# Performance work log

Measured on AMD Instinct MI355X. Metric: run time of the kernel, lower is better.

## Reference

```python
import jax, jax.numpy as jnp
import numpy as np

N_ATOMS = 200_000
AVG_NEIGHBORS = 64
N_PAIRS = N_ATOMS * AVG_NEIGHBORS
BOX = 60.0  # Angstrom, so cutoff=10 masks most random pairs (realistic neighbor-list sparsity)


def setup_inputs() -> dict:
    key = jax.random.key(0)
    kR, ki, kj = jax.random.split(key, 3)
    R = jax.random.uniform(kR, (N_ATOMS, 3), dtype=jnp.float32) * BOX
    idx_i = jax.random.randint(ki, (N_PAIRS,), 0, N_ATOMS, dtype=jnp.int32)
    idx_j = jax.random.randint(kj, (N_PAIRS,), 0, N_ATOMS, dtype=jnp.int32)
    # learned scalar parameters from __init__
    epsilon = jnp.float32(0.238)
    sigma = jnp.float32(3.4)
    cutoff = jnp.float32(10.0)
    return {"R": R, "epsilon": epsilon, "sigma": sigma, "cutoff": cutoff,
            "idx_i": idx_i, "idx_j": idx_j}


def reference(R, epsilon, sigma, cutoff, idx_i, idx_j):
    """LJ 12-6 pairwise potential over a neighbor list.

    Returns (energy [N] per-atom, forces [N,3]).
    Each (i,j) pair appears in both directions in the pair list, hence the 0.5
    factor on per-atom energy; forces accumulate per direction (action-reaction
    handled by the symmetric pair list).
    """
    n_atoms = R.shape[0]
    rij = R[idx_i] - R[idx_j]                     # [P,3] gather
    r2 = jnp.sum(rij * rij, axis=-1)              # [P]
    mask = (r2 < cutoff * cutoff) & (r2 > 1e-10)  # inside cutoff, exclude coincident
    r2s = jnp.where(mask, r2, 1.0)                # safe divide
    sr2 = (sigma * sigma) / r2s
    sr6 = sr2 * sr2 * sr2
    sr12 = sr6 * sr6
    e_pair = jnp.where(mask, 4.0 * epsilon * (sr12 - sr6), 0.0)          # [P]
    f_mag = jnp.where(mask, 24.0 * epsilon * (2.0 * sr12 - sr6) / r2s, 0.0)
    f_pair = f_mag[:, None] * rij                 # [P,3]
    energy = 0.5 * jax.ops.segment_sum(e_pair, idx_i, num_segments=n_atoms)   # [N]
    forces = jax.ops.segment_sum(f_pair, idx_i, num_segments=n_atoms)         # [N,3]
    return energy, forces
```

## Files before the change

kernel.cpp:

```cpp
#include <hip/hip_runtime.h>


typedef int   v4i __attribute__((ext_vector_type(4)));
typedef float v4f __attribute__((ext_vector_type(4)));

#define GRP    8
#define WGT    1024
#define NWG_F  256

__global__ void __launch_bounds__(256) prep_kernel(
    const float* __restrict__ R, const float* __restrict__ cut_p,
    v4f* __restrict__ Rp, unsigned* __restrict__ packed, int n_atoms)
{
    int t = blockIdx.x * blockDim.x + threadIdx.x;
    int n_grp = (n_atoms + 4) / 5;
    if (t >= n_grp) return;
    const float inv_cut = 1.0f / cut_p[0];
    int a0 = t * 5;
    unsigned w = 0u;
#pragma unroll
    for (int k = 0; k < 5; ++k) {
        int a = a0 + k;
        if (a < n_atoms) {
            float x = R[3 * a + 0];
            float y = R[3 * a + 1];
            float z = R[3 * a + 2];
            v4f v; v.x = x; v.y = y; v.z = z; v.w = 0.0f;
            Rp[a] = v;
            int cx = min(7, max(0, (int)(x * inv_cut)));
            int cy = min(7, max(0, (int)(y * inv_cut)));
            w |= (unsigned)(cx | (cy << 3)) << (6 * k);
        }
    }
    packed[t] = w;
}

__global__ void __launch_bounds__(256) pad_R_kernel(
    const float* __restrict__ R, v4f* __restrict__ Rp, int n_atoms)
{
    int a = blockIdx.x * blockDim.x + threadIdx.x;
    if (a < n_atoms) {
        v4f v;
        v.x = R[3 * a + 0];
        v.y = R[3 * a + 1];
        v.z = R[3 * a + 2];
        v.w = 0.0f;
        Rp[a] = v;
    }
}

__device__ __forceinline__ unsigned cell6w(const unsigned* __restrict__ lds32,
                                           unsigned a) {
    unsigned q = __umulhi(a, 0xCCCCCCCDu) >> 2;
    unsigned r = a - q * 5u;
    return (lds32[q] >> (r * 6u)) & 63u;
}

__device__ __forceinline__ void load_grp(
    const int* __restrict__ idx_i, const int* __restrict__ idx_j,
    int p, int n_pairs, int* __restrict__ is8, int* __restrict__ js8)
{
    if (p + GRP <= n_pairs) {
        v4i a0 = __builtin_nontemporal_load((const v4i*)idx_i + (p >> 2));
        v4i a1 = __builtin_nontemporal_load((const v4i*)idx_i + (p >> 2) + 1);
        v4i b0 = __builtin_nontemporal_load((const v4i*)idx_j + (p >> 2));
        v4i b1 = __builtin_nontemporal_load((const v4i*)idx_j + (p >> 2) + 1);
        is8[0] = a0.x; is8[1] = a0.y; is8[2] = a0.z; is8[3] = a0.w;
        is8[4] = a1.x; is8[5] = a1.y; is8[6] = a1.z; is8[7] = a1.w;
        js8[0] = b0.x; js8[1] = b0.y; js8[2] = b0.z; js8[3] = b0.w;
        js8[4] = b1.x; js8[5] = b1.y; js8[6] = b1.z; js8[7] = b1.w;
    } else {
#pragma unroll
        for (int k = 0; k < GRP; ++k) {
            bool v = (p + k < n_pairs);
            is8[k] = v ? idx_i[p + k] : 0;
            js8[k] = v ? idx_j[p + k] : 0;
        }
    }
}

__device__ __forceinline__ void filt_sel(const unsigned* __restrict__ lds32,
                                         int* __restrict__ is8,
                                         int* __restrict__ js8)
{
#pragma unroll
    for (int k = 0; k < GRP; ++k) {
        unsigned ci = cell6w(lds32, (unsigned)is8[k]);
        unsigned cj = cell6w(lds32, (unsigned)js8[k]);
        int ddx = (int)(ci & 7u) - (int)(cj & 7u);
        int ddy = (int)(ci >> 3) - (int)(cj >> 3);
        bool ok = ((unsigned)(ddx + 1) <= 2u) & ((unsigned)(ddy + 1) <= 2u);
        is8[k] = ok ? is8[k] : 0;
        js8[k] = ok ? js8[k] : 0;
    }
}

__device__ __forceinline__ void lj_body(
    v4f A, v4f B, float eps, float s2, float cut2, int gi,
    float* __restrict__ energy, float* __restrict__ forces)
{
    const float dx = A.x - B.x, dy = A.y - B.y, dz = A.z - B.z;
    const float r2 = dx * dx + dy * dy + dz * dz;
    if (r2 < cut2 && r2 > 1e-10f) {
        const float inv  = 1.0f / r2;
        const float sr2  = s2 * inv;
        const float sr6  = sr2 * sr2 * sr2;
        const float sr12 = sr6 * sr6;
        const float e    = 2.0f * eps * (sr12 - sr6);
        const float f    = 24.0f * eps * (2.0f * sr12 - sr6) * inv;
        atomicAdd(&energy[gi], e);
        atomicAdd(&forces[3 * gi + 0], f * dx);
        atomicAdd(&forces[3 * gi + 1], f * dy);
        atomicAdd(&forces[3 * gi + 2], f * dz);
    }
}

__global__ void __launch_bounds__(WGT, 4) lj_fused_kernel(
    const v4f* __restrict__ Rp,
    const unsigned* __restrict__ packed,
    const int* __restrict__ idx_i,
    const int* __restrict__ idx_j,
    const float* __restrict__ eps_p,
    const float* __restrict__ sig_p,
    const float* __restrict__ cut_p,
    float* __restrict__ energy,
    float* __restrict__ forces,
    int n_pairs, int pk_words, int chunk)
{
    extern __shared__ unsigned lds[];
    for (int w = threadIdx.x; w < pk_words; w += WGT)
        lds[w] = packed[w];
    __syncthreads();

    const float eps  = eps_p[0];
    const float sig  = sig_p[0];
    const float cut  = cut_p[0];
    const float s2   = sig * sig;
    const float cut2 = cut * cut;

    const int cs = blockIdx.x * chunk;
    const int ce = min(cs + chunk, n_pairs);
    const int STRIDE = WGT * GRP;

    int p0 = cs + (int)threadIdx.x * GRP;
    if (p0 >= ce) return;

    int isA[GRP], jsA[GRP], isB[GRP], jsB[GRP];

    load_grp(idx_i, idx_j, p0, n_pairs, isA, jsA);
    filt_sel(lds, isA, jsA);
    int p1 = p0 + STRIDE;

    while (true) {
        const bool h1 = p1 < ce;

        if (h1) load_grp(idx_i, idx_j, p1, n_pairs, isB, jsB);

        v4f Ri[GRP], Rj[GRP];
#pragma unroll
        for (int k = 0; k < GRP; ++k) { Ri[k] = Rp[isA[k]]; Rj[k] = Rp[jsA[k]]; }

        if (h1) filt_sel(lds, isB, jsB);

#pragma unroll
        for (int k = 0; k < GRP; ++k)
            lj_body(Ri[k], Rj[k], eps, s2, cut2, isA[k], energy, forces);

        if (!h1) break;
#pragma unroll
        for (int k = 0; k < GRP; ++k) { isA[k] = isB[k]; jsA[k] = jsB[k]; }
        p1 += STRIDE;
    }
}

#define PPT 8
__global__ void __launch_bounds__(256) lj_pairs_fb_kernel(
    const v4f* __restrict__ Rp,
    const v4i* __restrict__ idx_i4, const v4i* __restrict__ idx_j4,
    const float* __restrict__ eps_p, const float* __restrict__ sig_p,
    const float* __restrict__ cut_p,
    float* __restrict__ energy, float* __restrict__ forces, int n_oct)
{
    int t = blockIdx.x * blockDim.x + threadIdx.x;
    if (t >= n_oct) return;
    const float eps  = eps_p[0];
    const float sig  = sig_p[0];
    const float cut  = cut_p[0];
    const float s2   = sig * sig;
    const float cut2 = cut * cut;
    v4i ii0 = __builtin_nontemporal_load(idx_i4 + 2 * t);
    v4i ii1 = __builtin_nontemporal_load(idx_i4 + 2 * t + 1);
    v4i jj0 = __builtin_nontemporal_load(idx_j4 + 2 * t);
    v4i jj1 = __builtin_nontemporal_load(idx_j4 + 2 * t + 1);
    int is[PPT] = { ii0.x, ii0.y, ii0.z, ii0.w, ii1.x, ii1.y, ii1.z, ii1.w };
    int js[PPT] = { jj0.x, jj0.y, jj0.z, jj0.w, jj1.x, jj1.y, jj1.z, jj1.w };
    v4f Ri[PPT], Rj[PPT];
#pragma unroll
    for (int k = 0; k < PPT; ++k) Ri[k] = Rp[is[k]];
#pragma unroll
    for (int k = 0; k < PPT; ++k) Rj[k] = Rp[js[k]];
#pragma unroll
    for (int k = 0; k < PPT; ++k)
        lj_body(Ri[k], Rj[k], eps, s2, cut2, is[k], energy, forces);
}

__global__ void lj_pairs_fb_tail_kernel(
    const v4f* __restrict__ Rp,
    const int* __restrict__ idx_i, const int* __restrict__ idx_j,
    const float* __restrict__ eps_p, const float* __restrict__ sig_p,
    const float* __restrict__ cut_p,
    float* __restrict__ energy, float* __restrict__ forces,
    int start, int n_pairs)
{
    int p = start + blockIdx.x * blockDim.x + threadIdx.x;
    if (p >= n_pairs) return;
    const float eps = eps_p[0];
    const float sig = sig_p[0];
    const float cut = cut_p[0];
    lj_body(Rp[idx_i[p]], Rp[idx_j[p]], eps, sig * sig, cut * cut,
            idx_i[p], energy, forces);
}

extern "C" void kernel_launch(void* const* d_in, const int* in_sizes, int n_in,
                              void* d_out, int out_size, void* d_ws, size_t ws_size,
                              hipStream_t stream) {
    const float* R     = (const float*)d_in[0];
    const float* eps_p = (const float*)d_in[1];
    const float* sig_p = (const float*)d_in[2];
    const float* cut_p = (const float*)d_in[3];
    const int*   idx_i = (const int*)d_in[4];
    const int*   idx_j = (const int*)d_in[5];

    const int n_atoms = in_sizes[0] / 3;
    const int n_pairs = in_sizes[4];

    float* energy = (float*)d_out;
    float* forces = (float*)d_out + n_atoms;

    (void)hipMemsetAsync(d_out, 0, (size_t)out_size * sizeof(float), stream);

    char* ws = (char*)d_ws;
    const size_t rp_b     = (((size_t)n_atoms * 16) + 255) & ~(size_t)255;
    const int    pk_words = (n_atoms + 4) / 5;
    const size_t pk_b     = (((size_t)pk_words * 4) + 255) & ~(size_t)255;
    const size_t lds_b    = (((size_t)pk_words * 4) + 15) & ~(size_t)15;

    const bool have_rp    = ws_size >= rp_b;
    const bool use_filter = have_rp && (ws_size >= rp_b + pk_b)
                            && (lds_b <= 160000);

    v4f*      Rp     = (v4f*)ws;
    unsigned* packed = (unsigned*)(ws + rp_b);

    if (use_filter) {
        int pblocks = (pk_words + 255) / 256;
        prep_kernel<<<pblocks, 256, 0, stream>>>(R, cut_p, Rp, packed, n_atoms);

        (void)hipFuncSetAttribute((const void*)lj_fused_kernel,
                                  hipFuncAttributeMaxDynamicSharedMemorySize,
                                  (int)lds_b);

        int chunk = (((n_pairs + NWG_F - 1) / NWG_F) + GRP - 1) & ~(GRP - 1);
        lj_fused_kernel<<<NWG_F, WGT, lds_b, stream>>>(
            Rp, packed, idx_i, idx_j, eps_p, sig_p, cut_p,
            energy, forces, n_pairs, pk_words, chunk);
    } else if (have_rp) {
        int blocks = (n_atoms + 255) / 256;
        pad_R_kernel<<<blocks, 256, 0, stream>>>(R, Rp, n_atoms);
        const int n_oct = n_pairs / PPT;
        const int start = n_oct * PPT;
        if (n_oct > 0) {
            int fblocks = (n_oct + 255) / 256;
            lj_pairs_fb_kernel<<<fblocks, 256, 0, stream>>>(
                Rp, (const v4i*)idx_i, (const v4i*)idx_j,
                eps_p, sig_p, cut_p, energy, forces, n_oct);
        }
        if (start < n_pairs) {
            lj_pairs_fb_tail_kernel<<<1, 64, 0, stream>>>(
                Rp, idx_i, idx_j, eps_p, sig_p, cut_p,
                energy, forces, start, n_pairs);
        }
    }
}
```

Before: 188.5 us.

## Split fused LJ kernel into cell-filter compaction pass and dense compute pass

```diff
diff --git a/kernel.cpp b/kernel.cpp
--- a/kernel.cpp
+++ b/kernel.cpp
@@ -7,6 +7,8 @@
 #define GRP    8
 #define WGT    1024
 #define NWG_F  256
+#define CWG    512
+#define QUAD   4
 
 __global__ void __launch_bounds__(256) prep_kernel(
     const float* __restrict__ R, const float* __restrict__ cut_p,
@@ -76,22 +78,6 @@
             is8[k] = v ? idx_i[p + k] : 0;
             js8[k] = v ? idx_j[p + k] : 0;
         }
-    }
-}
-
-__device__ __forceinline__ void filt_sel(const unsigned* __restrict__ lds32,
-                                         int* __restrict__ is8,
-                                         int* __restrict__ js8)
-{
-#pragma unroll
-    for (int k = 0; k < GRP; ++k) {
-        unsigned ci = cell6w(lds32, (unsigned)is8[k]);
-        unsigned cj = cell6w(lds32, (unsigned)js8[k]);
-        int ddx = (int)(ci & 7u) - (int)(cj & 7u);
-        int ddy = (int)(ci >> 3) - (int)(cj >> 3);
-        bool ok = ((unsigned)(ddx + 1) <= 2u) & ((unsigned)(ddy + 1) <= 2u);
-        is8[k] = ok ? is8[k] : 0;
-        js8[k] = ok ? js8[k] : 0;
     }
 }
 
@@ -115,6 +101,141 @@
     }
 }
 
+__global__ void __launch_bounds__(WGT) filter_compact_kernel(
+    const unsigned* __restrict__ packed,
+    const int* __restrict__ idx_i,
+    const int* __restrict__ idx_j,
+    int2* __restrict__ list,
+    int* __restrict__ counts,
+    int n_pairs, int pk_words, int chunk)
+{
+    extern __shared__ unsigned lds[];
+    unsigned* blk_cnt = &lds[pk_words];
+    for (int w = threadIdx.x; w < pk_words; w += WGT)
+        lds[w] = packed[w];
+    if (threadIdx.x == 0) *blk_cnt = 0u;
+    __syncthreads();
+
+    const int g  = blockIdx.x;
+    const int cs = g * chunk;
+    const int ce = min(cs + chunk, n_pairs);
+    const int STRIDE = WGT * GRP;
+    const int n_iter = (ce > cs) ? (ce - cs + STRIDE - 1) / STRIDE : 0;
+
+    int2* out = list + (size_t)g * (size_t)chunk;
+
+    int p = cs + (int)threadIdx.x * GRP;
+    for (int it = 0; it < n_iter; ++it, p += STRIDE) {
+        const bool v = p < ce;
+        int is8[GRP], js8[GRP];
+        unsigned m = 0u;
+        if (v) {
+            load_grp(idx_i, idx_j, p, n_pairs, is8, js8);
+#pragma unroll
+            for (int k = 0; k < GRP; ++k) {
+                unsigned ci = cell6w(lds, (unsigned)is8[k]);
+                unsigned cj = cell6w(lds, (unsigned)js8[k]);
+                int ddx = (int)(ci & 7u) - (int)(cj & 7u);
+                int ddy = (int)(ci >> 3) - (int)(cj >> 3);
+                bool ok = ((unsigned)(ddx + 1) <= 2u) &
+                          ((unsigned)(ddy + 1) <= 2u);
+                if (ok) m |= (1u << k);
+            }
+        }
+
+        int tot = 0;
+        int pre[GRP];
+#pragma unroll
+        for (int k = 0; k < GRP; ++k) {
+            unsigned long long bal = __ballot((m >> k) & 1u);
+            int before = __builtin_amdgcn_mbcnt_hi(
+                (unsigned)(bal >> 32),
+                __builtin_amdgcn_mbcnt_lo((unsigned)bal, 0u));
+            pre[k] = tot + before;
+            tot   += (int)__popcll(bal);
+        }
+
+        unsigned wb = 0u;
+        if ((threadIdx.x & 63u) == 0u)
+            wb = atomicAdd(blk_cnt, (unsigned)tot);
+        wb = (unsigned)__shfl((int)wb, 0, 64);
+
+#pragma unroll
+        for (int k = 0; k < GRP; ++k)
+            if ((m >> k) & 1u) {
+                int2 pr; pr.x = is8[k]; pr.y = js8[k];
+                out[wb + (unsigned)pre[k]] = pr;
+            }
+    }
+
+    __syncthreads();
+    if (threadIdx.x == 0) counts[g] = (int)*blk_cnt;
+}
+
+__global__ void __launch_bounds__(CWG, 8) lj_compute_kernel(
+    const v4f* __restrict__ Rp,
+    const int2* __restrict__ list,
+    const int* __restrict__ counts,
+    const float* __restrict__ eps_p,
+    const float* __restrict__ sig_p,
+    const float* __restrict__ cut_p,
+    float* __restrict__ energy,
+    float* __restrict__ forces,
+    int chunk)
+{
+    const int g   = blockIdx.x >> 2;
+    const int q   = blockIdx.x & (QUAD - 1);
+    const int cnt = counts[g];
+    const int qn  = (cnt + QUAD - 1) >> 2;
+    const int s   = q * qn;
+    const int e   = min(cnt, s + qn);
+    if (s >= e) return;
+
+    const int2* seg = list + (size_t)g * (size_t)chunk;
+
+    const float eps  = eps_p[0];
+    const float sig  = sig_p[0];
+    const float cut  = cut_p[0];
+    const float s2   = sig * sig;
+    const float cut2 = cut * cut;
+
+#define GRP2 4
+    for (int b = s + (int)threadIdx.x * GRP2; b < e; b += CWG * GRP2) {
+        int2 pr[GRP2];
+#pragma unroll
+        for (int k = 0; k < GRP2; ++k) {
+            if (b + k < e) pr[k] = seg[b + k];
+            else { pr[k].x = 0; pr[k].y = 0; }
+        }
+        v4f Ri[GRP2], Rj[GRP2];
+#pragma unroll
+        for (int k = 0; k < GRP2; ++k) {
+            Ri[k] = Rp[pr[k].x];
+            Rj[k] = Rp[pr[k].y];
+        }
+#pragma unroll
+        for (int k = 0; k < GRP2; ++k)
+            lj_body(Ri[k], Rj[k], eps, s2, cut2, pr[k].x, energy, forces);
+    }
+#undef GRP2
+}
+
+__device__ __forceinline__ void filt_sel(const unsigned* __restrict__ lds32,
+                                         int* __restrict__ is8,
+                                         int* __restrict__ js8)
+{
+#pragma unroll
+    for (int k = 0; k < GRP; ++k) {
+        unsigned ci = cell6w(lds32, (unsigned)is8[k]);
+        unsigned cj = cell6w(lds32, (unsigned)js8[k]);
+        int ddx = (int)(ci & 7u) - (int)(cj & 7u);
+        int ddy = (int)(ci >> 3) - (int)(cj >> 3);
+        bool ok = ((unsigned)(ddx + 1) <= 2u) & ((unsigned)(ddy + 1) <= 2u);
+        is8[k] = ok ? is8[k] : 0;
+        js8[k] = ok ? js8[k] : 0;
+    }
+}
+
 __global__ void __launch_bounds__(WGT, 4) lj_fused_kernel(
     const v4f* __restrict__ Rp,
     const unsigned* __restrict__ packed,
@@ -146,26 +267,20 @@
     if (p0 >= ce) return;
 
     int isA[GRP], jsA[GRP], isB[GRP], jsB[GRP];
-
     load_grp(idx_i, idx_j, p0, n_pairs, isA, jsA);
     filt_sel(lds, isA, jsA);
     int p1 = p0 + STRIDE;
 
     while (true) {
         const bool h1 = p1 < ce;
-
         if (h1) load_grp(idx_i, idx_j, p1, n_pairs, isB, jsB);
-
         v4f Ri[GRP], Rj[GRP];
 #pragma unroll
         for (int k = 0; k < GRP; ++k) { Ri[k] = Rp[isA[k]]; Rj[k] = Rp[jsA[k]]; }
-
         if (h1) filt_sel(lds, isB, jsB);
-
 #pragma unroll
         for (int k = 0; k < GRP; ++k)
             lj_body(Ri[k], Rj[k], eps, s2, cut2, isA[k], energy, forces);
-
         if (!h1) break;
 #pragma unroll
         for (int k = 0; k < GRP; ++k) { isA[k] = isB[k]; jsA[k] = jsB[k]; }
@@ -243,24 +358,43 @@
     const size_t rp_b     = (((size_t)n_atoms * 16) + 255) & ~(size_t)255;
     const int    pk_words = (n_atoms + 4) / 5;
     const size_t pk_b     = (((size_t)pk_words * 4) + 255) & ~(size_t)255;
-    const size_t lds_b    = (((size_t)pk_words * 4) + 15) & ~(size_t)15;
+    const size_t ct_b     = (((size_t)NWG_F * 4) + 255) & ~(size_t)255;
+    const int    chunk    = (((n_pairs + NWG_F - 1) / NWG_F) + GRP - 1)
+                            & ~(GRP - 1);
+    const size_t li_b     = (size_t)NWG_F * (size_t)chunk * 8;
+    const size_t lds_b    = (((size_t)(pk_words + 1) * 4) + 15) & ~(size_t)15;
 
     const bool have_rp    = ws_size >= rp_b;
-    const bool use_filter = have_rp && (ws_size >= rp_b + pk_b)
-                            && (lds_b <= 160000);
+    const bool lds_ok     = lds_b <= 160 * 1024;
+    const bool use_split  = have_rp && lds_ok
+                            && (ws_size >= rp_b + pk_b + ct_b + li_b);
+    const bool use_filter = !use_split && have_rp && lds_ok
+                            && (ws_size >= rp_b + pk_b);
 
     v4f*      Rp     = (v4f*)ws;
     unsigned* packed = (unsigned*)(ws + rp_b);
-
-    if (use_filter) {
+    int*      counts = (int*)(ws + rp_b + pk_b);
+    int2*     list   = (int2*)(ws + rp_b + pk_b + ct_b);
+
+    if (use_split) {
         int pblocks = (pk_words + 255) / 256;
         prep_kernel<<<pblocks, 256, 0, stream>>>(R, cut_p, Rp, packed, n_atoms);
 
+        (void)hipFuncSetAttribute((const void*)filter_compact_kernel,
+                                  hipFuncAttributeMaxDynamicSharedMemorySize,
+                                  (int)lds_b);
+        filter_compact_kernel<<<NWG_F, WGT, lds_b, stream>>>(
+            packed, idx_i, idx_j, list, counts, n_pairs, pk_words, chunk);
+
+        lj_compute_kernel<<<NWG_F * QUAD, CWG, 0, stream>>>(
+            Rp, list, counts, eps_p, sig_p, cut_p, energy, forces, chunk);
+    } else if (use_filter) {
+        int pblocks = (pk_words + 255) / 256;
+        prep_kernel<<<pblocks, 256, 0, stream>>>(R, cut_p, Rp, packed, n_atoms);
+
         (void)hipFuncSetAttribute((const void*)lj_fused_kernel,
                                   hipFuncAttributeMaxDynamicSharedMemorySize,
-                                  (int)lds_b);
-
-        int chunk = (((n_pairs + NWG_F - 1) / NWG_F) + GRP - 1) & ~(GRP - 1);
+                                  (int)(lds_b));
         lj_fused_kernel<<<NWG_F, WGT, lds_b, stream>>>(
             Rp, packed, idx_i, idx_j, eps_p, sig_p, cut_p,
             energy, forces, n_pairs, pk_words, chunk);
```

Result: slower. 202.6 us (+7.5%).

## Split cell filter into Y-compaction pass and XZ-filtered LJ pass

Applied to the files above, without the earlier changes.

```diff
diff --git a/kernel.cpp b/kernel.cpp
--- a/kernel.cpp
+++ b/kernel.cpp
@@ -4,9 +4,45 @@
 typedef int   v4i __attribute__((ext_vector_type(4)));
 typedef float v4f __attribute__((ext_vector_type(4)));
 
-#define GRP    8
-#define WGT    1024
-#define NWG_F  256
+#define GRP     8
+#define WGT     1024
+#define K1_NWG  512
+#define K2_NWG  256
+#define NWG_F   256
+
+__global__ void __launch_bounds__(256) prep3_kernel(
+    const float* __restrict__ R, const float* __restrict__ cut_p,
+    v4f* __restrict__ Rp, unsigned* __restrict__ packedY,
+    unsigned* __restrict__ packedXZ, int n_atoms)
+{
+    int t = blockIdx.x * blockDim.x + threadIdx.x;
+    int n_grp = (n_atoms + 9) / 10;
+    if (t >= n_grp) return;
+    const float inv_cut = 1.0f / cut_p[0];
+    int a0 = t * 10;
+    unsigned wy = 0u, wxz0 = 0u, wxz1 = 0u;
+#pragma unroll
+    for (int k = 0; k < 10; ++k) {
+        int a = a0 + k;
+        if (a < n_atoms) {
+            float x = R[3 * a + 0];
+            float y = R[3 * a + 1];
+            float z = R[3 * a + 2];
+            v4f v; v.x = x; v.y = y; v.z = z; v.w = 0.0f;
+            Rp[a] = v;
+            unsigned cx = (unsigned)min(7, max(0, (int)(x * inv_cut)));
+            unsigned cy = (unsigned)min(7, max(0, (int)(y * inv_cut)));
+            unsigned cz = (unsigned)min(7, max(0, (int)(z * inv_cut)));
+            wy |= cy << (3 * k);
+            unsigned cxz = cx | (cz << 3);
+            if (k < 5) wxz0 |= cxz << (6 * k);
+            else       wxz1 |= cxz << (6 * (k - 5));
+        }
+    }
+    packedY[t]          = wy;
+    packedXZ[2 * t]     = wxz0;
+    packedXZ[2 * t + 1] = wxz1;
+}
 
 __global__ void __launch_bounds__(256) prep_kernel(
     const float* __restrict__ R, const float* __restrict__ cut_p,
@@ -49,6 +85,13 @@
     }
 }
 
+__device__ __forceinline__ unsigned cell3w(const unsigned* __restrict__ lds32,
+                                           unsigned a) {
+    unsigned q = __umulhi(a, 0xCCCCCCCDu) >> 3;
+    unsigned r = a - q * 10u;
+    return (lds32[q] >> (r * 3u)) & 7u;
+}
+
 __device__ __forceinline__ unsigned cell6w(const unsigned* __restrict__ lds32,
                                            unsigned a) {
     unsigned q = __umulhi(a, 0xCCCCCCCDu) >> 2;
@@ -76,22 +119,6 @@
             is8[k] = v ? idx_i[p + k] : 0;
             js8[k] = v ? idx_j[p + k] : 0;
         }
-    }
-}
-
-__device__ __forceinline__ void filt_sel(const unsigned* __restrict__ lds32,
-                                         int* __restrict__ is8,
-                                         int* __restrict__ js8)
-{
-#pragma unroll
-    for (int k = 0; k < GRP; ++k) {
-        unsigned ci = cell6w(lds32, (unsigned)is8[k]);
-        unsigned cj = cell6w(lds32, (unsigned)js8[k]);
-        int ddx = (int)(ci & 7u) - (int)(cj & 7u);
-        int ddy = (int)(ci >> 3) - (int)(cj >> 3);
-        bool ok = ((unsigned)(ddx + 1) <= 2u) & ((unsigned)(ddy + 1) <= 2u);
-        is8[k] = ok ? is8[k] : 0;
-        js8[k] = ok ? js8[k] : 0;
     }
 }
 
@@ -115,6 +142,147 @@
     }
 }
 
+__global__ void __launch_bounds__(WGT, 8) filter_y_kernel(
+    const unsigned* __restrict__ packedY,
+    const int* __restrict__ idx_i,
+    const int* __restrict__ idx_j,
+    int2* __restrict__ list,
+    int* __restrict__ count,
+    int n_pairs, int pk3_words)
+{
+    extern __shared__ unsigned lds[];
+    for (int w = threadIdx.x; w < pk3_words; w += WGT)
+        lds[w] = packedY[w];
+    __syncthreads();
+
+    const int stride = (int)gridDim.x * WGT * GRP;
+    int p = ((int)blockIdx.x * WGT + (int)threadIdx.x) * GRP;
+    const int n_iter = (n_pairs + stride - 1) / stride;
+
+    for (int it = 0; it < n_iter; ++it, p += stride) {
+        const bool v = p < n_pairs;
+        int is8[GRP], js8[GRP];
+        unsigned m = 0u;
+        if (v) {
+            load_grp(idx_i, idx_j, p, n_pairs, is8, js8);
+#pragma unroll
+            for (int k = 0; k < GRP; ++k) {
+                int dd = (int)cell3w(lds, (unsigned)is8[k])
+                       - (int)cell3w(lds, (unsigned)js8[k]);
+                if ((unsigned)(dd + 1) <= 2u) m |= (1u << k);
+            }
+        }
+
+        int tot = 0;
+        int pre[GRP];
+#pragma unroll
+        for (int k = 0; k < GRP; ++k) {
+            unsigned long long bal = __ballot((m >> k) & 1u);
+            int before = __builtin_amdgcn_mbcnt_hi(
+                (unsigned)(bal >> 32),
+                __builtin_amdgcn_mbcnt_lo((unsigned)bal, 0u));
+            pre[k] = tot + before;
+            tot   += (int)__popcll(bal);
+        }
+
+        int wb = 0;
+        if (tot > 0) {
+            if ((threadIdx.x & 63u) == 0u)
+                wb = atomicAdd(count, tot);
+            wb = __shfl(wb, 0, 64);
+#pragma unroll
+            for (int k = 0; k < GRP; ++k)
+                if ((m >> k) & 1u) {
+                    int2 pr; pr.x = is8[k]; pr.y = js8[k];
+                    list[wb + pre[k]] = pr;
+                }
+        }
+    }
+}
+
+__global__ void __launch_bounds__(WGT, 4) lj_xz_kernel(
+    const v4f* __restrict__ Rp,
+    const unsigned* __restrict__ packedXZ,
+    const int2* __restrict__ list,
+    const int* __restrict__ count,
+    const float* __restrict__ eps_p,
+    const float* __restrict__ sig_p,
+    const float* __restrict__ cut_p,
+    float* __restrict__ energy,
+    float* __restrict__ forces,
+    int pkxz_words)
+{
+    extern __shared__ unsigned lds[];
+    for (int w = threadIdx.x; w < pkxz_words; w += WGT)
+        lds[w] = packedXZ[w];
+    __syncthreads();
+
+    const int   cnt  = *count;
+    const float eps  = eps_p[0];
+    const float sig  = sig_p[0];
+    const float cut  = cut_p[0];
+    const float s2   = sig * sig;
+    const float cut2 = cut * cut;
+
+    const int stride = (int)gridDim.x * WGT * GRP;
+
+    for (int b = ((int)blockIdx.x * WGT + (int)threadIdx.x) * GRP;
+         b < cnt; b += stride) {
+        int2 pr[GRP];
+        if (b + GRP <= cnt) {
+            v4i q0 = __builtin_nontemporal_load((const v4i*)list + (b >> 1));
+            v4i q1 = __builtin_nontemporal_load((const v4i*)list + (b >> 1) + 1);
+            v4i q2 = __builtin_nontemporal_load((const v4i*)list + (b >> 1) + 2);
+            v4i q3 = __builtin_nontemporal_load((const v4i*)list + (b >> 1) + 3);
+            pr[0].x = q0.x; pr[0].y = q0.y; pr[1].x = q0.z; pr[1].y = q0.w;
+            pr[2].x = q1.x; pr[2].y = q1.y; pr[3].x = q1.z; pr[3].y = q1.w;
+            pr[4].x = q2.x; pr[4].y = q2.y; pr[5].x = q2.z; pr[5].y = q2.w;
+            pr[6].x = q3.x; pr[6].y = q3.y; pr[7].x = q3.z; pr[7].y = q3.w;
+        } else {
+#pragma unroll
+            for (int k = 0; k < GRP; ++k) {
+                if (b + k < cnt) pr[k] = list[b + k];
+                else { pr[k].x = 0; pr[k].y = 0; }
+            }
+        }
+
+#pragma unroll
+        for (int k = 0; k < GRP; ++k) {
+            unsigned ci = cell6w(lds, (unsigned)pr[k].x);
+            unsigned cj = cell6w(lds, (unsigned)pr[k].y);
+            int ddx = (int)(ci & 7u) - (int)(cj & 7u);
+            int ddz = (int)(ci >> 3) - (int)(cj >> 3);
+            bool ok = ((unsigned)(ddx + 1) <= 2u) & ((unsigned)(ddz + 1) <= 2u);
+            pr[k].x = ok ? pr[k].x : 0;
+            pr[k].y = ok ? pr[k].y : 0;
+        }
+
+        v4f Ri[GRP], Rj[GRP];
+#pragma unroll
+        for (int k = 0; k < GRP; ++k) { Ri[k] = Rp[pr[k].x]; Rj[k] = Rp[pr[k].y]; }
+
+#pragma unroll
+        for (int k = 0; k < GRP; ++k)
+            lj_body(Ri[k], Rj[k], eps, s2, cut2, pr[k].x, energy, forces);
+    }
+}
+
+__device__ __forceinline__ void filt_sel(const unsigned* __restrict__ lds32,
+                                         int* __restrict__ is8,
+                                         int* __restrict__ js8)
+{
+#pragma unroll
+    for (int k = 0; k < GRP; ++k) {
+        unsigned ci = cell6w(lds32, (unsigned)is8[k]);
+        unsigned cj = cell6w(lds32, (unsigned)js8[k]);
+        int ddx = (int)(ci & 7u) - (int)(cj & 7u);
+        int ddy = (int)(ci >> 3) - (int)(cj >> 3);
+        bool ok = ((unsigned)(ddx + 1) <= 2u) & ((unsigned)(ddy + 1) <= 2u);
+        is8[k] = ok ? is8[k] : 0;
+        js8[k] = ok ? js8[k] : 0;
+    }
+}
+
 __global__ void __launch_bounds__(WGT, 4) lj_fused_kernel(
     const v4f* __restrict__ Rp,
     const unsigned* __restrict__ packed,
@@ -146,26 +314,20 @@
     if (p0 >= ce) return;
 
     int isA[GRP], jsA[GRP], isB[GRP], jsB[GRP];
-
     load_grp(idx_i, idx_j, p0, n_pairs, isA, jsA);
     filt_sel(lds, isA, jsA);
     int p1 = p0 + STRIDE;
 
     while (true) {
         const bool h1 = p1 < ce;
-
         if (h1) load_grp(idx_i, idx_j, p1, n_pairs, isB, jsB);
-
         v4f Ri[GRP], Rj[GRP];
 #pragma unroll
         for (int k = 0; k < GRP; ++k) { Ri[k] = Rp[isA[k]]; Rj[k] = Rp[jsA[k]]; }
-
         if (h1) filt_sel(lds, isB, jsB);
-
 #pragma unroll
         for (int k = 0; k < GRP; ++k)
             lj_body(Ri[k], Rj[k], eps, s2, cut2, isA[k], energy, forces);
-
         if (!h1) break;
 #pragma unroll
         for (int k = 0; k < GRP; ++k) { isA[k] = isB[k]; jsA[k] = jsB[k]; }
@@ -240,31 +402,68 @@
     (void)hipMemsetAsync(d_out, 0, (size_t)out_size * sizeof(float), stream);
 
     char* ws = (char*)d_ws;
-    const size_t rp_b     = (((size_t)n_atoms * 16) + 255) & ~(size_t)255;
-    const int    pk_words = (n_atoms + 4) / 5;
-    const size_t pk_b     = (((size_t)pk_words * 4) + 255) & ~(size_t)255;
-    const size_t lds_b    = (((size_t)pk_words * 4) + 15) & ~(size_t)15;
-
-    const bool have_rp    = ws_size >= rp_b;
-    const bool use_filter = have_rp && (ws_size >= rp_b + pk_b)
-                            && (lds_b <= 160000);
-
-    v4f*      Rp     = (v4f*)ws;
-    unsigned* packed = (unsigned*)(ws + rp_b);
-
-    if (use_filter) {
+    const size_t rp_b       = (((size_t)n_atoms * 16) + 255) & ~(size_t)255;
+    const int    pk3_words  = (n_atoms + 9) / 10;
+    const int    pkxz_words = 2 * pk3_words;
+    const size_t pk3_b      = (((size_t)pk3_words * 4) + 255) & ~(size_t)255;
+    const size_t pkxz_b     = (((size_t)pkxz_words * 4) + 255) & ~(size_t)255;
+    const size_t cnt_b      = 256;
+    const size_t list_b     = (size_t)n_pairs * 8;
+    const size_t ldsY_b     = (((size_t)pk3_words * 4) + 15) & ~(size_t)15;
+    const size_t ldsXZ_b    = (((size_t)pkxz_words * 4) + 15) & ~(size_t)15;
+
+    const int    pk_words   = (n_atoms + 4) / 5;
+    const size_t pk_b       = (((size_t)pk_words * 4) + 255) & ~(size_t)255;
+    const size_t ldsF_b     = (((size_t)pk_words * 4) + 15) & ~(size_t)15;
+
+    const bool have_rp   = ws_size >= rp_b;
+    const bool use_split = have_rp
+        && (ldsY_b <= 160 * 1024) && (ldsXZ_b <= 160 * 1024)
+        && (ws_size >= rp_b + pk3_b + pkxz_b + cnt_b + list_b);
+    const bool use_fused = !use_split && have_rp
+        && (ldsF_b <= 160 * 1024) && (ws_size >= rp_b + pk_b);
+
+    if (use_split) {
+        v4f*      Rp       = (v4f*)ws;
+        unsigned* packedY  = (unsigned*)(ws + rp_b);
+        unsigned* packedXZ = (unsigned*)(ws + rp_b + pk3_b);
+        int*      count    = (int*)(ws + rp_b + pk3_b + pkxz_b);
+        int2*     list     = (int2*)(ws + rp_b + pk3_b + pkxz_b + cnt_b);
+
+        (void)hipMemsetAsync(count, 0, sizeof(int), stream);
+
+        int pblocks = ((n_atoms + 9) / 10 + 255) / 256;
+        prep3_kernel<<<pblocks, 256, 0, stream>>>(
+            R, cut_p, Rp, packedY, packedXZ, n_atoms);
+
+        (void)hipFuncSetAttribute((const void*)filter_y_kernel,
+                                  hipFuncAttributeMaxDynamicSharedMemorySize,
+                                  (int)ldsY_b);
+        filter_y_kernel<<<K1_NWG, WGT, ldsY_b, stream>>>(
+            packedY, idx_i, idx_j, list, count, n_pairs, pk3_words);
+
+        (void)hipFuncSetAttribute((const void*)lj_xz_kernel,
+                                  hipFuncAttributeMaxDynamicSharedMemorySize,
+                                  (int)ldsXZ_b);
+        lj_xz_kernel<<<K2_NWG, WGT, ldsXZ_b, stream>>>(
+            Rp, packedXZ, list, count, eps_p, sig_p, cut_p,
+            energy, forces, pkxz_words);
+    } else if (use_fused) {
+        v4f*      Rp     = (v4f*)ws;
+        unsigned* packed = (unsigned*)(ws + rp_b);
+
         int pblocks = (pk_words + 255) / 256;
         prep_kernel<<<pblocks, 256, 0, stream>>>(R, cut_p, Rp, packed, n_atoms);
 
         (void)hipFuncSetAttribute((const void*)lj_fused_kernel,
                                   hipFuncAttributeMaxDynamicSharedMemorySize,
-                                  (int)lds_b);
-
+                                  (int)ldsF_b);
         int chunk = (((n_pairs + NWG_F - 1) / NWG_F) + GRP - 1) & ~(GRP - 1);
-        lj_fused_kernel<<<NWG_F, WGT, lds_b, stream>>>(
+        lj_fused_kernel<<<NWG_F, WGT, ldsF_b, stream>>>(
             Rp, packed, idx_i, idx_j, eps_p, sig_p, cut_p,
             energy, forces, n_pairs, pk_words, chunk);
     } else if (have_rp) {
+        v4f* Rp = (v4f*)ws;
         int blocks = (n_atoms + 255) / 256;
         pad_R_kernel<<<blocks, 256, 0, stream>>>(R, Rp, n_atoms);
         const int n_oct = n_pairs / PPT;
```

Result: slower. 466.3 us (+147.4%).

## Accumulate energy and forces into padded float4 staging buffer with packed atomics

Applied to the files above, without the earlier changes.

```diff
diff --git a/kernel.cpp b/kernel.cpp
--- a/kernel.cpp
+++ b/kernel.cpp
@@ -1,12 +1,27 @@
 #include <hip/hip_runtime.h>
+#include <stdint.h>
 
 
 typedef int   v4i __attribute__((ext_vector_type(4)));
 typedef float v4f __attribute__((ext_vector_type(4)));
+typedef float v2f __attribute__((ext_vector_type(2)));
 
 #define GRP    8
 #define WGT    1024
 #define NWG_F  256
+
+#if __has_builtin(__builtin_amdgcn_global_atomic_fadd_v2f32)
+__device__ __forceinline__ void pk_atomic_add(float* p, float a, float b) {
+    typedef __attribute__((address_space(1))) v2f gv2f;
+    v2f v; v.x = a; v.y = b;
+    (void)__builtin_amdgcn_global_atomic_fadd_v2f32((gv2f*)(uintptr_t)p, v);
+}
+#else
+__device__ __forceinline__ void pk_atomic_add(float* p, float a, float b) {
+    atomicAdd(p, a);
+    atomicAdd(p + 1, b);
+}
+#endif
 
 __global__ void __launch_bounds__(256) prep_kernel(
     const float* __restrict__ R, const float* __restrict__ cut_p,
@@ -92,6 +107,25 @@
         bool ok = ((unsigned)(ddx + 1) <= 2u) & ((unsigned)(ddy + 1) <= 2u);
         is8[k] = ok ? is8[k] : 0;
         js8[k] = ok ? js8[k] : 0;
+    }
+}
+
+__device__ __forceinline__ void lj_body_st(
+    v4f A, v4f B, float eps, float s2, float cut2, int gi,
+    float* __restrict__ st)
+{
+    const float dx = A.x - B.x, dy = A.y - B.y, dz = A.z - B.z;
+    const float r2 = dx * dx + dy * dy + dz * dz;
+    if (r2 < cut2 && r2 > 1e-10f) {
+        const float inv  = 1.0f / r2;
+        const float sr2  = s2 * inv;
+        const float sr6  = sr2 * sr2 * sr2;
+        const float sr12 = sr6 * sr6;
+        const float e    = 2.0f * eps * (sr12 - sr6);
+        const float f    = 24.0f * eps * (2.0f * sr12 - sr6) * inv;
+        float* p = st + ((size_t)(unsigned)gi << 2);
+        pk_atomic_add(p,     e,      f * dx);
+        pk_atomic_add(p + 2, f * dy, f * dz);
     }
 }
 
@@ -115,6 +149,77 @@
     }
 }
 
+__global__ void __launch_bounds__(WGT, 4) lj_fused_st_kernel(
+    const v4f* __restrict__ Rp,
+    const unsigned* __restrict__ packed,
+    const int* __restrict__ idx_i,
+    const int* __restrict__ idx_j,
+    const float* __restrict__ eps_p,
+    const float* __restrict__ sig_p,
+    const float* __restrict__ cut_p,
+    float* __restrict__ st,
+    int n_pairs, int pk_words, int chunk)
+{
+    extern __shared__ unsigned lds[];
+    for (int w = threadIdx.x; w < pk_words; w += WGT)
+        lds[w] = packed[w];
+    __syncthreads();
+
+    const float eps  = eps_p[0];
+    const float sig  = sig_p[0];
+    const float cut  = cut_p[0];
+    const float s2   = sig * sig;
+    const float cut2 = cut * cut;
+
+    const int cs = blockIdx.x * chunk;
+    const int ce = min(cs + chunk, n_pairs);
+    const int STRIDE = WGT * GRP;
+
+    int p0 = cs + (int)threadIdx.x * GRP;
+    if (p0 >= ce) return;
+
+    int isA[GRP], jsA[GRP], isB[GRP], jsB[GRP];
+
+    load_grp(idx_i, idx_j, p0, n_pairs, isA, jsA);
+    filt_sel(lds, isA, jsA);
+    int p1 = p0 + STRIDE;
+
+    while (true) {
+        const bool h1 = p1 < ce;
+
+        if (h1) load_grp(idx_i, idx_j, p1, n_pairs, isB, jsB);
+
+        v4f Ri[GRP], Rj[GRP];
+#pragma unroll
+        for (int k = 0; k < GRP; ++k) { Ri[k] = Rp[isA[k]]; Rj[k] = Rp[jsA[k]]; }
+
+        if (h1) filt_sel(lds, isB, jsB);
+
+#pragma unroll
+        for (int k = 0; k < GRP; ++k)
+            lj_body_st(Ri[k], Rj[k], eps, s2, cut2, isA[k], st);
+
+        if (!h1) break;
+#pragma unroll
+        for (int k = 0; k < GRP; ++k) { isA[k] = isB[k]; jsA[k] = jsB[k]; }
+        p1 += STRIDE;
+    }
+}
+
+__global__ void __launch_bounds__(256) finalize_kernel(
+    const v4f* __restrict__ st, float* __restrict__ energy,
+    float* __restrict__ forces, int n_atoms)
+{
+    int a = blockIdx.x * blockDim.x + threadIdx.x;
+    if (a < n_atoms) {
+        v4f s = st[a];
+        energy[a]          = s.x;
+        forces[3 * a + 0]  = s.y;
+        forces[3 * a + 1]  = s.z;
+        forces[3 * a + 2]  = s.w;
+    }
+}
+
 __global__ void __launch_bounds__(WGT, 4) lj_fused_kernel(
     const v4f* __restrict__ Rp,
     const unsigned* __restrict__ packed,
@@ -146,26 +251,20 @@
     if (p0 >= ce) return;
 
     int isA[GRP], jsA[GRP], isB[GRP], jsB[GRP];
-
     load_grp(idx_i, idx_j, p0, n_pairs, isA, jsA);
     filt_sel(lds, isA, jsA);
     int p1 = p0 + STRIDE;
 
     while (true) {
         const bool h1 = p1 < ce;
-
         if (h1) load_grp(idx_i, idx_j, p1, n_pairs, isB, jsB);
-
         v4f Ri[GRP], Rj[GRP];
 #pragma unroll
         for (int k = 0; k < GRP; ++k) { Ri[k] = Rp[isA[k]]; Rj[k] = Rp[jsA[k]]; }
-
         if (h1) filt_sel(lds, isB, jsB);
-
 #pragma unroll
         for (int k = 0; k < GRP; ++k)
             lj_body(Ri[k], Rj[k], eps, s2, cut2, isA[k], energy, forces);
-
         if (!h1) break;
 #pragma unroll
         for (int k = 0; k < GRP; ++k) { isA[k] = isB[k]; jsA[k] = jsB[k]; }
@@ -237,34 +336,57 @@
     float* energy = (float*)d_out;
     float* forces = (float*)d_out + n_atoms;
 
-    (void)hipMemsetAsync(d_out, 0, (size_t)out_size * sizeof(float), stream);
-
     char* ws = (char*)d_ws;
     const size_t rp_b     = (((size_t)n_atoms * 16) + 255) & ~(size_t)255;
     const int    pk_words = (n_atoms + 4) / 5;
     const size_t pk_b     = (((size_t)pk_words * 4) + 255) & ~(size_t)255;
+    const size_t st_b     = (((size_t)n_atoms * 16) + 255) & ~(size_t)255;
     const size_t lds_b    = (((size_t)pk_words * 4) + 15) & ~(size_t)15;
 
-    const bool have_rp    = ws_size >= rp_b;
-    const bool use_filter = have_rp && (ws_size >= rp_b + pk_b)
-                            && (lds_b <= 160000);
+    const bool have_rp  = ws_size >= rp_b;
+    const bool lds_ok   = lds_b <= 160000;
+    const bool use_st   = have_rp && lds_ok
+                          && (ws_size >= rp_b + pk_b + st_b);
+    const bool use_old  = !use_st && have_rp && lds_ok
+                          && (ws_size >= rp_b + pk_b);
 
     v4f*      Rp     = (v4f*)ws;
     unsigned* packed = (unsigned*)(ws + rp_b);
-
-    if (use_filter) {
+    float*    st     = (float*)(ws + rp_b + pk_b);
+
+    if (use_st) {
+        (void)hipMemsetAsync(st, 0, (size_t)n_atoms * 16, stream);
+
+        int pblocks = (pk_words + 255) / 256;
+        prep_kernel<<<pblocks, 256, 0, stream>>>(R, cut_p, Rp, packed, n_atoms);
+
+        (void)hipFuncSetAttribute((const void*)lj_fused_st_kernel,
+                                  hipFuncAttributeMaxDynamicSharedMemorySize,
+                                  (int)lds_b);
+        int chunk = (((n_pairs + NWG_F - 1) / NWG_F) + GRP - 1) & ~(GRP - 1);
+        lj_fused_st_kernel<<<NWG_F, WGT, lds_b, stream>>>(
+            Rp, packed, idx_i, idx_j, eps_p, sig_p, cut_p,
+            st, n_pairs, pk_words, chunk);
+
+        int fblocks = (n_atoms + 255) / 256;
+        finalize_kernel<<<fblocks, 256, 0, stream>>>(
+            (const v4f*)st, energy, forces, n_atoms);
+    } else if (use_old) {
+        (void)hipMemsetAsync(d_out, 0, (size_t)out_size * sizeof(float), stream);
+
         int pblocks = (pk_words + 255) / 256;
         prep_kernel<<<pblocks, 256, 0, stream>>>(R, cut_p, Rp, packed, n_atoms);
 
         (void)hipFuncSetAttribute((const void*)lj_fused_kernel,
                                   hipFuncAttributeMaxDynamicSharedMemorySize,
                                   (int)lds_b);
-
         int chunk = (((n_pairs + NWG_F - 1) / NWG_F) + GRP - 1) & ~(GRP - 1);
         lj_fused_kernel<<<NWG_F, WGT, lds_b, stream>>>(
             Rp, packed, idx_i, idx_j, eps_p, sig_p, cut_p,
             energy, forces, n_pairs, pk_words, chunk);
     } else if (have_rp) {
+        (void)hipMemsetAsync(d_out, 0, (size_t)out_size * sizeof(float), stream);
+
         int blocks = (n_atoms + 255) / 256;
         pad_R_kernel<<<blocks, 256, 0, stream>>>(R, Rp, n_atoms);
         const int n_oct = n_pairs / PPT;
```

Measured after the change: 191.0 us. About the same (+1.3%).
